# Kernel optimization log

Measured on AMD Instinct MI355X. Metric: run time of the kernel, lower is better.

Reference implementation:

```python
import jax, jax.numpy as jnp
import numpy as np
import math

ROPE_BASE = 10000.0

def rope(x):
    # rotate-half RoPE over the full feature dim. x: [B, S, D]
    B, S, D = x.shape
    half = D // 2
    inv_freq = 1.0 / (ROPE_BASE ** (jnp.arange(half, dtype=jnp.float32) / half))
    ang = jnp.arange(S, dtype=jnp.float32)[:, None] * inv_freq[None, :]  # [S, half]
    cos, sin = jnp.cos(ang), jnp.sin(ang)
    x1, x2 = x[..., :half], x[..., half:]
    return jnp.concatenate([x1 * cos - x2 * sin, x1 * sin + x2 * cos], axis=-1)

def setup_inputs() -> dict:
    key = jax.random.key(0)
    ks = jax.random.split(key, 10)
    B, S, D = 4, 2048, 2048
    scale = 1.0 / math.sqrt(D)
    x = jax.random.normal(ks[0], (B, S, D), dtype=jnp.float32)
    mask = jnp.broadcast_to(jnp.tril(jnp.ones((S, S), dtype=jnp.int32)), (B, S, S))
    Wq = jax.random.normal(ks[1], (D, D), dtype=jnp.float32) * scale
    bq = jax.random.normal(ks[2], (D,), dtype=jnp.float32) * 0.02
    Wk = jax.random.normal(ks[3], (D, D), dtype=jnp.float32) * scale
    bk = jax.random.normal(ks[4], (D,), dtype=jnp.float32) * 0.02
    Wv = jax.random.normal(ks[5], (D, D), dtype=jnp.float32) * scale
    bv = jax.random.normal(ks[6], (D,), dtype=jnp.float32) * 0.02
    Wo = jax.random.normal(ks[7], (D, D), dtype=jnp.float32) * scale
    bo = jax.random.normal(ks[8], (D,), dtype=jnp.float32) * 0.02
    return {"x": x, "mask": mask, "Wq": Wq, "bq": bq, "Wk": Wk, "bk": bk,
            "Wv": Wv, "bv": bv, "Wo": Wo, "bo": bo}

def reference(x, mask, Wq, bq, Wk, bk, Wv, bv, Wo, bo):
    # x: [B, S, D]; torch.nn.Linear convention: y = x @ W.T + b
    D = x.shape[-1]
    std = jnp.sqrt(jnp.asarray(D, dtype=x.dtype))
    q = jnp.einsum('bsd,ed->bse', x, Wq) + bq
    k = jnp.einsum('bsd,ed->bse', x, Wk) + bk
    v = jnp.einsum('bsd,ed->bse', x, Wv) + bv
    # cache=None prefill path: q sliced to last x.size(-2) positions (full seq here)
    Sq = x.shape[-2]
    q = rope(q)[:, -Sq:, :]
    k = rope(k)
    scores = jnp.einsum('bqd,bkd->bqk', q, k) / std  # [B, Sq, Sk]
    scores = jnp.where(mask[:, -Sq:, :] == 0, -jnp.inf, scores)
    attn = jax.nn.softmax(scores, axis=-1)  # dropout=0 (eval)
    ctx = jnp.einsum('bqk,bkd->bqd', attn, v)
    out = jnp.einsum('bqd,ed->bqe', ctx, Wo) + bo
    return out
```

## Files before the change

kernel.cpp:

```cpp
#include <hip/hip_runtime.h>
#include <stdint.h>
#include <math.h>

#define BLK 256

typedef __bf16 bf16x8 __attribute__((ext_vector_type(8)));
typedef float  f32x4  __attribute__((ext_vector_type(4)));

__device__ __forceinline__ uint16_t f2bf(float f) {
  uint32_t u = __float_as_uint(f);
  u += 0x7fffu + ((u >> 16) & 1u);
  return (uint16_t)(u >> 16);
}
__device__ __forceinline__ float bf2f(uint16_t h) {
  return __uint_as_float(((uint32_t)h) << 16);
}

__device__ __forceinline__ void load_lds16(const void* g, void* l) {
  __builtin_amdgcn_global_load_lds(
      (const __attribute__((address_space(1))) uint32_t*)g,
      (__attribute__((address_space(3))) uint32_t*)l,
      16, 0, 0);
}

__global__ __launch_bounds__(BLK)
void convert_all(const float* __restrict__ x, const float* __restrict__ wq,
                 const float* __restrict__ wk, const float* __restrict__ wv,
                 const float* __restrict__ wo,
                 uint16_t* __restrict__ xb, uint16_t* __restrict__ wqkv,
                 float* __restrict__ sums) {
  const long tid0 = (long)blockIdx.x * BLK + threadIdx.x;
  if (tid0 < 8192) sums[tid0] = 0.f;
  const long XG = 4194304;
  const long T  = XG + 4 * 1048576;
  for (long i = tid0; i < T; i += (long)gridDim.x * BLK) {
    const float* src; uint16_t* dst; long off, doff;
    if (i < XG) { src = x; dst = xb; off = i; doff = i; }
    else {
      const long j = i - XG;
      const int seg = (int)(j >> 20);
      off = j & 1048575;
      src = (seg == 0) ? wq : (seg == 1) ? wk : (seg == 2) ? wv : wo;
      dst = wqkv + ((long)seg << 22);
      if (seg < 2) {
        const int f = (int)(off >> 9);
        const int g = (int)(off & 511);
        const int c = (f < 1024) ? (f << 1) : (((f - 1024) << 1) | 1);
        doff = (long)c * 512 + g;
      } else doff = off;
    }
    float4 v = ((const float4*)src)[off];
    ushort4 o;
    o.x = f2bf(v.x); o.y = f2bf(v.y); o.z = f2bf(v.z); o.w = f2bf(v.w);
    ((ushort4*)dst)[doff] = o;
  }
}

template<int MODE, int MINW>
__global__ __launch_bounds__(BLK, MINW)
void gemm_bt(const uint16_t* __restrict__ A, int lda,
             const uint16_t* __restrict__ Bt, int ldb,
             const float* __restrict__ b0, const float* __restrict__ b1,
             const float* __restrict__ b2,
             void* __restrict__ Cv, int ldc,
             int K, long sAb, long sBb, long sCb,
             float scale, float* __restrict__ rowsum,
             uint16_t* __restrict__ Vt)
{
  int tile_m, tile_n, bz;
  if (MODE == 2) {
    const int t = blockIdx.x;
    int r = (int)((sqrtf(8.f * (float)t + 1.f) - 1.f) * 0.5f);
    while ((r + 1) * (r + 2) / 2 <= t) ++r;
    while (r * (r + 1) / 2 > t) --r;
    tile_m = r * 128;
    tile_n = (t - r * (r + 1) / 2) * 128;
    bz = blockIdx.z;
  } else if (MODE == 3) {
    bz = blockIdx.y & 3;
    tile_m = ((int)(gridDim.y >> 2) - 1 - (int)(blockIdx.y >> 2)) * 128;
    tile_n = blockIdx.x * 128;
  } else {
    tile_m = blockIdx.y * 128;
    tile_n = blockIdx.x * 128;
    bz = blockIdx.z;
  }
  A  += (long)bz * sAb;
  Bt += (long)bz * sBb;

  __shared__ __align__(16) uint16_t smem[16384];
  uint16_t* sA = smem;
  uint16_t* sB = smem + 8192;

  const int tid  = threadIdx.x;
  const int lane = tid & 63;
  const int wave = tid >> 6;
  const int quad = lane >> 4;
  const int l16  = lane & 15;
  const int x8   = l16 & 7;
  const int wm = (wave & 1) * 64;
  const int wn = (wave >> 1) * 64;

  f32x4 acc[4][4];
#pragma unroll
  for (int i = 0; i < 4; ++i)
#pragma unroll
    for (int j = 0; j < 4; ++j) acc[i][j] = (f32x4){0.f, 0.f, 0.f, 0.f};

  const uint16_t* gA[4]; const uint16_t* gB[4];
  uint16_t* lA[4]; uint16_t* lB[4];
#pragma unroll
  for (int i = 0; i < 4; ++i) {
    const int id = wave * 256 + i * 64 + lane;
    const int row = id >> 3;
    const int c = (id & 7) ^ (row & 7);
    gA[i] = A  + (long)(tile_m + row) * lda + c * 8;
    gB[i] = Bt + (long)(tile_n + row) * ldb + c * 8;
    lA[i] = sA + (wave * 256 + i * 64) * 8;
    lB[i] = sB + (wave * 256 + i * 64) * 8;
  }

  const int kend = (MODE == 3) ? min(K, tile_m + 128) : K;

  for (int kk = 0; kk < kend; kk += 64) {
#pragma unroll
    for (int i = 0; i < 4; ++i) {
      load_lds16(gA[i] + kk, lA[i]);
      load_lds16(gB[i] + kk, lB[i]);
    }
    __syncthreads();

#pragma unroll
    for (int s2 = 0; s2 < 2; ++s2) {
      const int slot = ((quad + s2 * 4) ^ x8) * 8;
      bf16x8 af[4], bfr[4];
#pragma unroll
      for (int mi = 0; mi < 4; ++mi)
        af[mi] = *(const bf16x8*)(sA + (wm + mi * 16 + l16) * 64 + slot);
#pragma unroll
      for (int ni = 0; ni < 4; ++ni)
        bfr[ni] = *(const bf16x8*)(sB + (wn + ni * 16 + l16) * 64 + slot);
#pragma unroll
      for (int mi = 0; mi < 4; ++mi)
#pragma unroll
        for (int ni = 0; ni < 4; ++ni)
          acc[mi][ni] = __builtin_amdgcn_mfma_f32_16x16x32_bf16(af[mi], bfr[ni], acc[mi][ni], 0, 0, 0);
    }
    __syncthreads();
  }

  const int crow0 = tile_m + wm + quad * 4;
  const int ccol0 = tile_n + wn + l16;

  if constexpr (MODE == 2) {
    const bool diag = (tile_m == tile_n);
    uint16_t* Pp = (uint16_t*)Cv + (long)bz * sCb;
    float* rs = rowsum + (long)bz * 2048;
#pragma unroll
    for (int mi = 0; mi < 4; ++mi) {
#pragma unroll
      for (int r = 0; r < 4; ++r) {
        const int row = crow0 + mi * 16 + r;
        float partial = 0.f;
#pragma unroll
        for (int ni = 0; ni < 4; ++ni) {
          const int col = ccol0 + ni * 16;
          const float e = (!diag || col <= row) ? __expf(acc[mi][ni][r] * scale) : 0.f;
          const uint16_t h = f2bf(e);
          partial += bf2f(h);
          Pp[(long)row * ldc + col] = h;
        }
#pragma unroll
        for (int o = 1; o < 16; o <<= 1) partial += __shfl_xor(partial, o, 64);
        if (l16 == 0) atomicAdd(rs + row, partial);
      }
    }
  } else if constexpr (MODE == 3) {
    uint16_t* Cp = (uint16_t*)Cv + (long)bz * sCb;
    const float* rs = rowsum + (long)bz * 2048;
#pragma unroll
    for (int mi = 0; mi < 4; ++mi) {
#pragma unroll
      for (int r = 0; r < 4; ++r) {
        const int row = crow0 + mi * 16 + r;
        const float inv = 1.f / rs[row];
#pragma unroll
        for (int ni = 0; ni < 4; ++ni)
          Cp[(long)row * ldc + ccol0 + ni * 16] = f2bf(acc[mi][ni][r] * inv);
      }
    }
  } else if constexpr (MODE == 1) {
    const int seg = tile_n >> 11;
    if (seg < 2) {
      const float* bp = seg ? b1 : b0;
      uint16_t* Cp = (uint16_t*)Cv;
#pragma unroll
      for (int ni = 0; ni < 4; ++ni) {
        const int col = ccol0 + ni * 16;
        const int cc = col & 2047;
        const float bb = bp[(cc >> 1) + (cc & 1) * 1024];
        const float invf = exp2f((float)(cc >> 1) * (-13.287712379549449f / 1024.f));
        const float sgn = (cc & 1) ? 1.f : -1.f;
#pragma unroll
        for (int mi = 0; mi < 4; ++mi) {
#pragma unroll
          for (int r = 0; r < 4; ++r) {
            const int row = crow0 + mi * 16 + r;
            const float v = acc[mi][ni][r] + bb;
            float sn, cs;
            __sincosf((float)(row & 2047) * invf, &sn, &cs);
            const float p = __shfl_xor(v, 1, 64);
            Cp[(long)row * 4096 + col] = f2bf(v * cs + p * sgn * sn);
          }
        }
      }
    } else {
#pragma unroll
      for (int ni = 0; ni < 4; ++ni) {
        const int cl = wn + l16 + ni * 16;
        const float bb = b2[(ccol0 + ni * 16) & 2047];
#pragma unroll
        for (int mi = 0; mi < 4; ++mi) {
          const int rl0 = wm + quad * 4 + mi * 16;
          union { uint16_t u16[4]; uint64_t u64; } pk;
#pragma unroll
          for (int r = 0; r < 4; ++r) pk.u16[r] = f2bf(acc[mi][ni][r] + bb);
          *(uint64_t*)(smem + cl * 128 + (rl0 ^ ((cl & 15) << 3))) = pk.u64;
        }
      }
      __syncthreads();
      const int fl = quad;
      const int t0 = l16 * 8;
      const int bno = tile_m >> 11;
      const int tokbase = tile_m & 2047;
      uint16_t* Vp = Vt + (long)bno * 4194304 + tokbase;
      const int featbase = tile_n - 4096;
#pragma unroll
      for (int jj = 0; jj < 8; ++jj) {
        const int c = jj * 16 + wave * 4 + fl;
        const uint16_t* srcp = smem + c * 128 + (t0 ^ ((c & 15) << 3));
        ulonglong2 v = *(const ulonglong2*)srcp;
        *(ulonglong2*)(Vp + (long)(featbase + c) * 2048 + t0) = v;
      }
    }
  } else {
#pragma unroll
    for (int ni = 0; ni < 4; ++ni) {
      const int col = ccol0 + ni * 16;
      const float bb = b0[col];
#pragma unroll
      for (int mi = 0; mi < 4; ++mi) {
#pragma unroll
        for (int r = 0; r < 4; ++r) {
          const long row = crow0 + mi * 16 + r;
          ((float*)Cv)[row * (long)ldc + col] = acc[mi][ni][r] * scale + bb;
        }
      }
    }
  }
}

extern "C" void kernel_launch(void* const* d_in, const int* in_sizes, int n_in,
                              void* d_out, int out_size, void* d_ws, size_t ws_size,
                              hipStream_t stream) {
  const long S = 2048, D = 2048;
  const long MD = 4 * S * D;
  const long DD = D * D;

  const float* x  = (const float*)d_in[0];
  const float* Wq = (const float*)d_in[2];
  const float* bq = (const float*)d_in[3];
  const float* Wk = (const float*)d_in[4];
  const float* bk = (const float*)d_in[5];
  const float* Wv = (const float*)d_in[6];
  const float* bv = (const float*)d_in[7];
  const float* Wo = (const float*)d_in[8];
  const float* bo = (const float*)d_in[9];

  uint16_t* Xb    = (uint16_t*)d_ws;
  uint16_t* Wqkvb = Xb + MD;
  uint16_t* QK    = Wqkvb + 4 * DD;
  uint16_t* Vt    = QK + 8192L * 4096;
  uint16_t* P     = Vt + MD;
  float*    sums  = (float*)(P + 4 * S * S);
  if (ws_size < 268435456ull) return;

  dim3 blk(BLK);

  convert_all<<<16384, blk, 0, stream>>>(x, Wq, Wk, Wv, Wo, Xb, Wqkvb, sums);

  gemm_bt<1, 4><<<dim3(48, 64, 1), blk, 0, stream>>>(
      Xb, 2048, Wqkvb, 2048, bq, bk, bv, QK, 4096,
      2048, 0, 0, 0, 1.f, nullptr, Vt);

  gemm_bt<2, 4><<<dim3(136, 1, 4), blk, 0, stream>>>(
      QK, 4096, QK + 2048, 4096, nullptr, nullptr, nullptr, P, 2048,
      2048, 2048L * 4096, 2048L * 4096, S * S,
      0.022097086912079608f, sums, nullptr);

  gemm_bt<3, 4><<<dim3(16, 64, 1), blk, 0, stream>>>(
      P, 2048, Vt, 2048, nullptr, nullptr, nullptr, Xb, 2048,
      2048, S * S, S * D, S * D, 1.f, sums, nullptr);

  gemm_bt<0, 4><<<dim3(16, 64, 1), blk, 0, stream>>>(
      Xb, 2048, Wqkvb + 3 * DD, 2048, bo, nullptr, nullptr, (float*)d_out, 2048,
      2048, 0, 0, 0, 1.f, nullptr, nullptr);
}
```

Measured before the change: 583.1 us.

## Use dedicated 64x128-tile causal QK^T kernel with finer triangular work split

Replaces the templated 128x128 triangular QK^T+exp stage with a dedicated kernel using 64-row by 128-column tiles. Blocks above the causal diagonal exit early, and strips are issued largest first. The smaller tiles waste less work on diagonal blocks and give more blocks for load balance, at the cost of lower reuse per tile and more blocks that launch only to return. Occupancy goes up to 5 blocks per unit with less shared memory per block.

```diff
diff --git a/kernel.cpp b/kernel.cpp
--- a/kernel.cpp
+++ b/kernel.cpp
@@ -56,6 +56,108 @@
   }
 }
 
+__global__ __launch_bounds__(BLK, 5)
+void qk_gemm(const uint16_t* __restrict__ Aall, const uint16_t* __restrict__ Ball,
+             uint16_t* __restrict__ Pall, float* __restrict__ rsall, float scale)
+{
+  const int strip = 31 - (int)blockIdx.y;
+  const int bz  = (int)blockIdx.x >> 4;
+  const int bxt = (int)blockIdx.x & 15;
+  if ((bxt << 1) > strip) return;
+  const int tile_m = strip << 6;
+  const int tile_n = bxt << 7;
+
+  const uint16_t* A  = Aall + (long)bz * (2048L * 4096);
+  const uint16_t* Bt = Ball + (long)bz * (2048L * 4096);
+  uint16_t* Pp = Pall + (long)bz * (2048L * 2048);
+  float*    rs = rsall + (long)bz * 2048;
+
+  __shared__ __align__(16) uint16_t smem[12288];
+  uint16_t* sA = smem;
+  uint16_t* sB = smem + 4096;
+
+  const int tid  = threadIdx.x;
+  const int lane = tid & 63;
+  const int wave = tid >> 6;
+  const int quad = lane >> 4;
+  const int l16  = lane & 15;
+  const int x8   = l16 & 7;
+  const int wn   = wave << 5;
+
+  f32x4 acc[4][2];
+#pragma unroll
+  for (int i = 0; i < 4; ++i)
+#pragma unroll
+    for (int j = 0; j < 2; ++j) acc[i][j] = (f32x4){0.f, 0.f, 0.f, 0.f};
+
+  const uint16_t* gA[2]; uint16_t* lA[2];
+  const uint16_t* gB[4]; uint16_t* lB[4];
+#pragma unroll
+  for (int i = 0; i < 2; ++i) {
+    const int id = wave * 128 + i * 64 + lane;
+    const int row = id >> 3;
+    const int c = (id & 7) ^ (row & 7);
+    gA[i] = A + (long)(tile_m + row) * 4096 + c * 8;
+    lA[i] = sA + (wave * 128 + i * 64) * 8;
+  }
+#pragma unroll
+  for (int i = 0; i < 4; ++i) {
+    const int id = wave * 256 + i * 64 + lane;
+    const int row = id >> 3;
+    const int c = (id & 7) ^ (row & 7);
+    gB[i] = Bt + (long)(tile_n + row) * 4096 + c * 8;
+    lB[i] = sB + (wave * 256 + i * 64) * 8;
+  }
+
+  for (int kk = 0; kk < 2048; kk += 64) {
+#pragma unroll
+    for (int i = 0; i < 2; ++i) load_lds16(gA[i] + kk, lA[i]);
+#pragma unroll
+    for (int i = 0; i < 4; ++i) load_lds16(gB[i] + kk, lB[i]);
+    __syncthreads();
+
+#pragma unroll
+    for (int s2 = 0; s2 < 2; ++s2) {
+      const int slot = ((quad + s2 * 4) ^ x8) * 8;
+      bf16x8 af[4], bfr[2];
+#pragma unroll
+      for (int mi = 0; mi < 4; ++mi)
+        af[mi] = *(const bf16x8*)(sA + (mi * 16 + l16) * 64 + slot);
+#pragma unroll
+      for (int ni = 0; ni < 2; ++ni)
+        bfr[ni] = *(const bf16x8*)(sB + (wn + ni * 16 + l16) * 64 + slot);
+#pragma unroll
+      for (int mi = 0; mi < 4; ++mi)
+#pragma unroll
+        for (int ni = 0; ni < 2; ++ni)
+          acc[mi][ni] = __builtin_amdgcn_mfma_f32_16x16x32_bf16(af[mi], bfr[ni], acc[mi][ni], 0, 0, 0);
+    }
+    __syncthreads();
+  }
+
+  const int crow0 = tile_m + quad * 4;
+  const int ccol0 = tile_n + wn + l16;
+#pragma unroll
+  for (int mi = 0; mi < 4; ++mi) {
+#pragma unroll
+    for (int r = 0; r < 4; ++r) {
+      const int row = crow0 + mi * 16 + r;
+      float partial = 0.f;
+#pragma unroll
+      for (int ni = 0; ni < 2; ++ni) {
+        const int col = ccol0 + ni * 16;
+        const float e = (col <= row) ? __expf(acc[mi][ni][r] * scale) : 0.f;
+        const uint16_t h = f2bf(e);
+        partial += bf2f(h);
+        Pp[(long)row * 2048 + col] = h;
+      }
+#pragma unroll
+      for (int o = 1; o < 16; o <<= 1) partial += __shfl_xor(partial, o, 64);
+      if (l16 == 0) atomicAdd(rs + row, partial);
+    }
+  }
+}
+
 template<int MODE, int MINW>
 __global__ __launch_bounds__(BLK, MINW)
 void gemm_bt(const uint16_t* __restrict__ A, int lda,
@@ -68,15 +170,7 @@
              uint16_t* __restrict__ Vt)
 {
   int tile_m, tile_n, bz;
-  if (MODE == 2) {
-    const int t = blockIdx.x;
-    int r = (int)((sqrtf(8.f * (float)t + 1.f) - 1.f) * 0.5f);
-    while ((r + 1) * (r + 2) / 2 <= t) ++r;
-    while (r * (r + 1) / 2 > t) --r;
-    tile_m = r * 128;
-    tile_n = (t - r * (r + 1) / 2) * 128;
-    bz = blockIdx.z;
-  } else if (MODE == 3) {
+  if (MODE == 3) {
     bz = blockIdx.y & 3;
     tile_m = ((int)(gridDim.y >> 2) - 1 - (int)(blockIdx.y >> 2)) * 128;
     tile_n = blockIdx.x * 128;
@@ -152,30 +246,7 @@
   const int crow0 = tile_m + wm + quad * 4;
   const int ccol0 = tile_n + wn + l16;
 
-  if constexpr (MODE == 2) {
-    const bool diag = (tile_m == tile_n);
-    uint16_t* Pp = (uint16_t*)Cv + (long)bz * sCb;
-    float* rs = rowsum + (long)bz * 2048;
-#pragma unroll
-    for (int mi = 0; mi < 4; ++mi) {
-#pragma unroll
-      for (int r = 0; r < 4; ++r) {
-        const int row = crow0 + mi * 16 + r;
-        float partial = 0.f;
-#pragma unroll
-        for (int ni = 0; ni < 4; ++ni) {
-          const int col = ccol0 + ni * 16;
-          const float e = (!diag || col <= row) ? __expf(acc[mi][ni][r] * scale) : 0.f;
-          const uint16_t h = f2bf(e);
-          partial += bf2f(h);
-          Pp[(long)row * ldc + col] = h;
-        }
-#pragma unroll
-        for (int o = 1; o < 16; o <<= 1) partial += __shfl_xor(partial, o, 64);
-        if (l16 == 0) atomicAdd(rs + row, partial);
-      }
-    }
-  } else if constexpr (MODE == 3) {
+  if constexpr (MODE == 3) {
     uint16_t* Cp = (uint16_t*)Cv + (long)bz * sCb;
     const float* rs = rowsum + (long)bz * 2048;
 #pragma unroll
@@ -293,10 +364,8 @@
       Xb, 2048, Wqkvb, 2048, bq, bk, bv, QK, 4096,
       2048, 0, 0, 0, 1.f, nullptr, Vt);
 
-  gemm_bt<2, 4><<<dim3(136, 1, 4), blk, 0, stream>>>(
-      QK, 4096, QK + 2048, 4096, nullptr, nullptr, nullptr, P, 2048,
-      2048, 2048L * 4096, 2048L * 4096, S * S,
-      0.022097086912079608f, sums, nullptr);
+  qk_gemm<<<dim3(64, 32, 1), blk, 0, stream>>>(
+      QK, QK + 2048, P, sums, 0.022097086912079608f);
 
   gemm_bt<3, 4><<<dim3(16, 64, 1), blk, 0, stream>>>(
       P, 2048, Vt, 2048, nullptr, nullptr, nullptr, Xb, 2048,
```

After: 604.8 us. 3.7% more time.
